# Optimization experiments

Hardware: AMD Instinct MI355X
Metric: run time of the kernel (lower is better)

Reference implementation:

```python
import jax, jax.numpy as jnp
import numpy as np

B, T, D, U = 32, 2048, 512, 512

def setup_inputs() -> dict:
    key = jax.random.key(0)
    ks = jax.random.split(key, 7)
    s = 1.0 / np.sqrt(D)
    return {
        "query": jax.random.normal(ks[0], (B, D), jnp.float32),
        "values": jax.random.normal(ks[1], (B, T, D), jnp.float32),
        "W1": jax.random.normal(ks[2], (D, U), jnp.float32) * s,
        "b1": jnp.zeros((U,), jnp.float32),
        "W2": jax.random.normal(ks[3], (D, U), jnp.float32) * s,
        "b2": jnp.zeros((U,), jnp.float32),
        "V": jax.random.normal(ks[4], (U, 1), jnp.float32) * (1.0 / np.sqrt(U)),
        "bV": jnp.zeros((1,), jnp.float32),
    }

def reference(query, values, W1, b1, W2, b2, V, bV):
    # values: [B,T,D], query: [B,D]
    proj_v = jnp.einsum('btd,du->btu', values, W1) + b1          # [B,T,U]
    proj_q = (query @ W2 + b2)[:, None, :]                        # [B,1,U]
    score = jnp.tanh(proj_v + proj_q) @ V + bV                    # [B,T,1]
    attention_weights = jax.nn.softmax(score, axis=1)             # [B,T,1]
    context_vector = jnp.sum(attention_weights * values, axis=1)  # [B,D]
    return (context_vector, attention_weights)
```

## Files before the change

### kernel.cpp

```cpp
#include <hip/hip_runtime.h>
#include <hip/hip_bf16.h>
#include <math.h>

#define BB 32
#define TT 2048
#define DD 512
#define UU 512

typedef __attribute__((ext_vector_type(8))) short short8v;
typedef __attribute__((ext_vector_type(4))) float floatx4;
typedef __attribute__((ext_vector_type(8))) unsigned short ushort8v;
typedef __attribute__((ext_vector_type(4))) unsigned short ushort4v;

static __device__ inline unsigned short f2bf(float f) {
  __hip_bfloat16 h = __float2bfloat16(f);
  return *reinterpret_cast<unsigned short*>(&h);
}

static __device__ inline float fast_tanh(float x) {
  x = fminf(fmaxf(x, -15.f), 15.f);
  float e2 = __expf(2.f * x);
  return (e2 - 1.f) * __builtin_amdgcn_rcpf(e2 + 1.f);
}

__global__ __launch_bounds__(256) void pack_w1a_kernel(
    const float* __restrict__ W1, unsigned short* __restrict__ w1a) {
  __shared__ float Wf[32][132];
  const int kt = blockIdx.x, uc = blockIdx.y;
  const int tid = threadIdx.x;
  {
    const int k = tid >> 3;
    const int u16 = (tid & 7) * 16;
    const float* src = W1 + (size_t)(kt * 32 + k) * UU + uc * 128 + u16;
    #pragma unroll
    for (int q = 0; q < 4; ++q) {
      const float4 v = *(const float4*)(src + q * 4);
      Wf[k][u16 + q * 4 + 0] = v.x;
      Wf[k][u16 + q * 4 + 1] = v.y;
      Wf[k][u16 + q * 4 + 2] = v.z;
      Wf[k][u16 + q * 4 + 3] = v.w;
    }
  }
  __syncthreads();
  unsigned short* dst = w1a + (size_t)kt * 16384;
  #pragma unroll
  for (int s = 0; s < 2; ++s) {
    const int c = s * 256 + tid;
    const int kg = c >> 7;
    const int u = c & 127;
    ushort8v o;
    #pragma unroll
    for (int e = 0; e < 8; ++e) o[e] = f2bf(Wf[kg * 8 + e][u]);
    *(ushort8v*)(dst + ((size_t)kg * 512 + uc * 128 + u) * 8) = o;
  }
}

__global__ __launch_bounds__(256) void projq_kernel(
    const float* __restrict__ query, const float* __restrict__ W2,
    const float* __restrict__ b2, const float* __restrict__ b1,
    float* __restrict__ qb) {
  int b = blockIdx.x;
  int u = blockIdx.y * 256 + threadIdx.x;
  float acc = b2[u] + b1[u];
  const float* q = query + b * DD;
  #pragma unroll 16
  for (int d = 0; d < DD; ++d) acc += q[d] * W2[(size_t)d * UU + u];
  qb[b * UU + u] = acc;
}

#define SBM 64

__global__ __launch_bounds__(512, 4) void score_fused_kernel(
    const float* __restrict__ values, const unsigned short* __restrict__ w1a,
    const float* __restrict__ qb, const float* __restrict__ V,
    float* __restrict__ score, float* __restrict__ o_part,
    float* __restrict__ l_part) {
  __shared__ __align__(16) unsigned short Bp[2][8][4][SBM][8];
  __shared__ float qv_lds[512];
  __shared__ float vv_lds[512];
  __shared__ float part[8][SBM];
  __shared__ float sw[SBM];
  __shared__ float opart[4][512];

  const int tid = threadIdx.x;
  const int row0 = blockIdx.x * SBM;
  const int b = row0 >> 11;
  const int lane = tid & 63;
  const int wid = tid >> 6;
  const int wu = wid * 64;
  const int fr = lane & 15;
  const int kg = lane >> 4;

  qv_lds[tid] = qb[b * UU + tid];
  vv_lds[tid] = V[tid];

  const int sm = tid >> 3;
  const int sj = tid & 7;
  const float* bsrc = values + (size_t)(row0 + sm) * DD + sj * 4;
  const int bofs = (sj >> 1) * (SBM * 8) + sm * 8 + (sj & 1) * 4;

  {
    float4 r0[8];
    #pragma unroll
    for (int q = 0; q < 8; ++q)
      r0[q] = *(const float4*)(bsrc + (size_t)q * 32);
    #pragma unroll
    for (int q = 0; q < 8; ++q) {
      ushort4v o = {f2bf(r0[q].x), f2bf(r0[q].y), f2bf(r0[q].z), f2bf(r0[q].w)};
      *(ushort4v*)(&Bp[0][q][0][0][0] + bofs) = o;
    }
  }

  const size_t aofs = (size_t)(kg * 512 + wu + fr) * 8;
  short8v af[3][4];
  #pragma unroll
  for (int ju = 0; ju < 4; ++ju) {
    af[0][ju] = *(const short8v*)(w1a + aofs + (size_t)ju * 128);
    af[1][ju] = *(const short8v*)(w1a + 16384 + aofs + (size_t)ju * 128);
  }

  __syncthreads();

  float4 r1[8];
  #pragma unroll
  for (int q = 0; q < 8; ++q)
    r1[q] = *(const float4*)(bsrc + (size_t)(8 + q) * 32);

  floatx4 acc[4][4] = {};

  #pragma unroll
  for (int t = 0; t < 16; ++t) {
    if (t == 8) {
      #pragma unroll
      for (int q = 0; q < 8; ++q) {
        ushort4v o = {f2bf(r1[q].x), f2bf(r1[q].y), f2bf(r1[q].z), f2bf(r1[q].w)};
        *(ushort4v*)(&Bp[1][q][0][0][0] + bofs) = o;
      }
      __syncthreads();
    }

    if (t + 2 < 16) {
      #pragma unroll
      for (int ju = 0; ju < 4; ++ju)
        af[(t + 2) % 3][ju] =
            *(const short8v*)(w1a + (size_t)(t + 2) * 16384 + aofs + (size_t)ju * 128);
    }

    #pragma unroll
    for (int jm = 0; jm < 4; ++jm) {
      const short8v bfv = *(const short8v*)&Bp[t >> 3][t & 7][kg][jm * 16 + fr][0];
      #pragma unroll
      for (int ju = 0; ju < 4; ++ju)
        acc[ju][jm] = __builtin_amdgcn_mfma_f32_16x16x32_bf16(af[t % 3][ju], bfv, acc[ju][jm], 0, 0, 0);
    }
  }

  float pm[4] = {0.f, 0.f, 0.f, 0.f};
  #pragma unroll
  for (int ju = 0; ju < 4; ++ju) {
    const float4 qv = *(const float4*)&qv_lds[wu + ju * 16 + kg * 4];
    const float4 vv = *(const float4*)&vv_lds[wu + ju * 16 + kg * 4];
    const float qa[4] = {qv.x, qv.y, qv.z, qv.w};
    const float va[4] = {vv.x, vv.y, vv.z, vv.w};
    #pragma unroll
    for (int jm = 0; jm < 4; ++jm)
      #pragma unroll
      for (int reg = 0; reg < 4; ++reg)
        pm[jm] += fast_tanh(acc[ju][jm][reg] + qa[reg]) * va[reg];
  }
  #pragma unroll
  for (int jm = 0; jm < 4; ++jm) {
    pm[jm] += __shfl_xor(pm[jm], 16, 64);
    pm[jm] += __shfl_xor(pm[jm], 32, 64);
  }
  if (lane < 16) {
    #pragma unroll
    for (int jm = 0; jm < 4; ++jm) part[wid][jm * 16 + lane] = pm[jm];
  }
  __syncthreads();
  if (tid < SBM) {
    float s = 0.f;
    #pragma unroll
    for (int w = 0; w < 8; ++w) s += part[w][tid];
    score[row0 + tid] = s;
    sw[tid] = __expf(s);
  }
  __syncthreads();

  {
    const int g = tid >> 7;
    const int dq = tid & 127;
    const float* vrow = values + (size_t)(row0 + g * 16) * DD + dq * 4;
    float4 o4 = {0.f, 0.f, 0.f, 0.f};
    #pragma unroll
    for (int r = 0; r < 16; ++r) {
      const float w = sw[g * 16 + r];
      const float4 v = *(const float4*)(vrow + (size_t)r * DD);
      o4.x += w * v.x; o4.y += w * v.y; o4.z += w * v.z; o4.w += w * v.w;
    }
    *(float4*)&opart[g][dq * 4] = o4;
  }
  if (wid == 0) {
    float lv = sw[lane];
    #pragma unroll
    for (int m = 1; m < 64; m <<= 1) lv += __shfl_xor(lv, m, 64);
    if (lane == 0) l_part[blockIdx.x] = lv;
  }
  __syncthreads();
  {
    const int d = tid;
    o_part[(size_t)blockIdx.x * DD + d] =
        opart[0][d] + opart[1][d] + opart[2][d] + opart[3][d];
  }
}

__global__ __launch_bounds__(128) void reduce_kernel(
    const float* __restrict__ o_part, const float* __restrict__ l_part,
    float* __restrict__ ctx, float* __restrict__ Linv) {
  const int b = blockIdx.x;
  const int d0 = threadIdx.x * 4;
  __shared__ float Ls;
  if (threadIdx.x == 0) {
    float s = 0.f;
    #pragma unroll 8
    for (int c = 0; c < 32; ++c) s += l_part[b * 32 + c];
    Ls = 1.f / s;
    Linv[b] = Ls;
  }
  float4 a = {0.f, 0.f, 0.f, 0.f};
  #pragma unroll 8
  for (int c = 0; c < 32; ++c) {
    const float4 p = *(const float4*)(o_part + (size_t)(b * 32 + c) * DD + d0);
    a.x += p.x; a.y += p.y; a.z += p.z; a.w += p.w;
  }
  __syncthreads();
  const float inv = Ls;
  a.x *= inv; a.y *= inv; a.z *= inv; a.w *= inv;
  *(float4*)(ctx + (size_t)b * DD + d0) = a;
}

__global__ __launch_bounds__(1024) void attn_kernel(
    const float* __restrict__ score, const float* __restrict__ Linv,
    float* __restrict__ attn) {
  const int i = blockIdx.x * 1024 + threadIdx.x;
  const int b = i >> 11;
  attn[i] = __expf(score[i]) * Linv[b];
}

extern "C" void kernel_launch(void* const* d_in, const int* in_sizes, int n_in,
                              void* d_out, int out_size, void* d_ws, size_t ws_size,
                              hipStream_t stream) {
  const float* query  = (const float*)d_in[0];
  const float* values = (const float*)d_in[1];
  const float* W1     = (const float*)d_in[2];
  const float* b1     = (const float*)d_in[3];
  const float* W2     = (const float*)d_in[4];
  const float* b2     = (const float*)d_in[5];
  const float* V      = (const float*)d_in[6];

  float* ctx  = (float*)d_out;
  float* attn = (float*)d_out + BB * DD;

  float* qb           = (float*)d_ws;
  float* score        = qb + BB * UU;
  unsigned short* w1a = (unsigned short*)(score + BB * TT);
  float* o_part       = (float*)(w1a + (size_t)UU * DD);
  float* l_part       = o_part + (size_t)1024 * DD;
  float* Linv         = l_part + 1024;

  pack_w1a_kernel<<<dim3(16, 4), 256, 0, stream>>>(W1, w1a);
  projq_kernel<<<dim3(BB, UU / 256), 256, 0, stream>>>(query, W2, b2, b1, qb);

  score_fused_kernel<<<(BB * TT) / SBM, 512, 0, stream>>>(
      values, w1a, qb, V, score, o_part, l_part);

  reduce_kernel<<<BB, 128, 0, stream>>>(o_part, l_part, ctx, Linv);
  attn_kernel<<<(BB * TT) / 1024, 1024, 0, stream>>>(score, Linv, attn);
}
```

Measured before the change: 86.50 us.

## Double score-kernel row tile to 128 and load all values up front

Each block of the fused score kernel now covers 128 rows instead of 64. Every W1 fragment fetched from global memory therefore feeds twice as many MFMAs, which halves W1 traffic per row and halves the number of partial outputs the reduce kernel has to combine. The mid-loop staging of the second half of values is gone: the full K slice is converted to bf16 in LDS before the loop, and the W1 prefetch depth drops from two steps to one. The cost is twice the LDS and accumulator registers per block and occupancy limited to 2 blocks per CU, with no overlap left between the values load and the MFMA work.

```diff
diff --git a/kernel.cpp b/kernel.cpp
--- a/kernel.cpp
+++ b/kernel.cpp
@@ -68,14 +68,14 @@
   qb[b * UU + u] = acc;
 }
 
-#define SBM 64
-
-__global__ __launch_bounds__(512, 4) void score_fused_kernel(
+#define SBM 128
+
+__global__ __launch_bounds__(512, 2) void score_fused_kernel(
     const float* __restrict__ values, const unsigned short* __restrict__ w1a,
     const float* __restrict__ qb, const float* __restrict__ V,
     float* __restrict__ score, float* __restrict__ o_part,
     float* __restrict__ l_part) {
-  __shared__ __align__(16) unsigned short Bp[2][8][4][SBM][8];
+  __shared__ __align__(16) unsigned short Bp[16][4][SBM][8];
   __shared__ float qv_lds[512];
   __shared__ float vv_lds[512];
   __shared__ float part[8][SBM];
@@ -94,68 +94,57 @@
   qv_lds[tid] = qb[b * UU + tid];
   vv_lds[tid] = V[tid];
 
-  const int sm = tid >> 3;
-  const int sj = tid & 7;
-  const float* bsrc = values + (size_t)(row0 + sm) * DD + sj * 4;
-  const int bofs = (sj >> 1) * (SBM * 8) + sm * 8 + (sj & 1) * 4;
-
-  {
-    float4 r0[8];
-    #pragma unroll
-    for (int q = 0; q < 8; ++q)
-      r0[q] = *(const float4*)(bsrc + (size_t)q * 32);
-    #pragma unroll
-    for (int q = 0; q < 8; ++q) {
-      ushort4v o = {f2bf(r0[q].x), f2bf(r0[q].y), f2bf(r0[q].z), f2bf(r0[q].w)};
-      *(ushort4v*)(&Bp[0][q][0][0][0] + bofs) = o;
+  {
+    const int sm = tid >> 2;
+    const int sj = tid & 3;
+    const float* bsrc = values + (size_t)(row0 + sm) * DD + sj * 4;
+    #pragma unroll
+    for (int batch = 0; batch < 4; ++batch) {
+      float4 r[8];
+      #pragma unroll
+      for (int i = 0; i < 8; ++i)
+        r[i] = *(const float4*)(bsrc + (size_t)(batch * 8 + i) * 16);
+      #pragma unroll
+      for (int i = 0; i < 8; ++i) {
+        const int f = sj * 4 + (batch * 8 + i) * 16;
+        const int kt = f >> 5;
+        const int kgw = (f >> 3) & 3;
+        const int e = f & 7;
+        ushort4v o = {f2bf(r[i].x), f2bf(r[i].y), f2bf(r[i].z), f2bf(r[i].w)};
+        *(ushort4v*)&Bp[kt][kgw][sm][e] = o;
+      }
     }
   }
 
   const size_t aofs = (size_t)(kg * 512 + wu + fr) * 8;
-  short8v af[3][4];
-  #pragma unroll
-  for (int ju = 0; ju < 4; ++ju) {
+  short8v af[2][4];
+  #pragma unroll
+  for (int ju = 0; ju < 4; ++ju)
     af[0][ju] = *(const short8v*)(w1a + aofs + (size_t)ju * 128);
-    af[1][ju] = *(const short8v*)(w1a + 16384 + aofs + (size_t)ju * 128);
-  }
-
-  __syncthreads();
-
-  float4 r1[8];
-  #pragma unroll
-  for (int q = 0; q < 8; ++q)
-    r1[q] = *(const float4*)(bsrc + (size_t)(8 + q) * 32);
-
-  floatx4 acc[4][4] = {};
+
+  __syncthreads();
+
+  floatx4 acc[4][8] = {};
 
   #pragma unroll
   for (int t = 0; t < 16; ++t) {
-    if (t == 8) {
-      #pragma unroll
-      for (int q = 0; q < 8; ++q) {
-        ushort4v o = {f2bf(r1[q].x), f2bf(r1[q].y), f2bf(r1[q].z), f2bf(r1[q].w)};
-        *(ushort4v*)(&Bp[1][q][0][0][0] + bofs) = o;
-      }
-      __syncthreads();
-    }
-
-    if (t + 2 < 16) {
+    const int cur = t & 1;
+    if (t + 1 < 16) {
       #pragma unroll
       for (int ju = 0; ju < 4; ++ju)
-        af[(t + 2) % 3][ju] =
-            *(const short8v*)(w1a + (size_t)(t + 2) * 16384 + aofs + (size_t)ju * 128);
-    }
-
-    #pragma unroll
-    for (int jm = 0; jm < 4; ++jm) {
-      const short8v bfv = *(const short8v*)&Bp[t >> 3][t & 7][kg][jm * 16 + fr][0];
+        af[cur ^ 1][ju] =
+            *(const short8v*)(w1a + (size_t)(t + 1) * 16384 + aofs + (size_t)ju * 128);
+    }
+    #pragma unroll
+    for (int jm = 0; jm < 8; ++jm) {
+      const short8v bfv = *(const short8v*)&Bp[t][kg][jm * 16 + fr][0];
       #pragma unroll
       for (int ju = 0; ju < 4; ++ju)
-        acc[ju][jm] = __builtin_amdgcn_mfma_f32_16x16x32_bf16(af[t % 3][ju], bfv, acc[ju][jm], 0, 0, 0);
-    }
-  }
-
-  float pm[4] = {0.f, 0.f, 0.f, 0.f};
+        acc[ju][jm] = __builtin_amdgcn_mfma_f32_16x16x32_bf16(af[cur][ju], bfv, acc[ju][jm], 0, 0, 0);
+    }
+  }
+
+  float pm[8] = {};
   #pragma unroll
   for (int ju = 0; ju < 4; ++ju) {
     const float4 qv = *(const float4*)&qv_lds[wu + ju * 16 + kg * 4];
@@ -163,19 +152,19 @@
     const float qa[4] = {qv.x, qv.y, qv.z, qv.w};
     const float va[4] = {vv.x, vv.y, vv.z, vv.w};
     #pragma unroll
-    for (int jm = 0; jm < 4; ++jm)
+    for (int jm = 0; jm < 8; ++jm)
       #pragma unroll
       for (int reg = 0; reg < 4; ++reg)
         pm[jm] += fast_tanh(acc[ju][jm][reg] + qa[reg]) * va[reg];
   }
   #pragma unroll
-  for (int jm = 0; jm < 4; ++jm) {
+  for (int jm = 0; jm < 8; ++jm) {
     pm[jm] += __shfl_xor(pm[jm], 16, 64);
     pm[jm] += __shfl_xor(pm[jm], 32, 64);
   }
   if (lane < 16) {
     #pragma unroll
-    for (int jm = 0; jm < 4; ++jm) part[wid][jm * 16 + lane] = pm[jm];
+    for (int jm = 0; jm < 8; ++jm) part[wid][jm * 16 + lane] = pm[jm];
   }
   __syncthreads();
   if (tid < SBM) {
@@ -190,18 +179,18 @@
   {
     const int g = tid >> 7;
     const int dq = tid & 127;
-    const float* vrow = values + (size_t)(row0 + g * 16) * DD + dq * 4;
+    const float* vrow = values + (size_t)(row0 + g * 32) * DD + dq * 4;
     float4 o4 = {0.f, 0.f, 0.f, 0.f};
-    #pragma unroll
-    for (int r = 0; r < 16; ++r) {
-      const float w = sw[g * 16 + r];
+    #pragma unroll 8
+    for (int r = 0; r < 32; ++r) {
+      const float w = sw[g * 32 + r];
       const float4 v = *(const float4*)(vrow + (size_t)r * DD);
       o4.x += w * v.x; o4.y += w * v.y; o4.z += w * v.z; o4.w += w * v.w;
     }
     *(float4*)&opart[g][dq * 4] = o4;
   }
   if (wid == 0) {
-    float lv = sw[lane];
+    float lv = sw[lane] + sw[lane + 64];
     #pragma unroll
     for (int m = 1; m < 64; m <<= 1) lv += __shfl_xor(lv, m, 64);
     if (lane == 0) l_part[blockIdx.x] = lv;
@@ -222,15 +211,15 @@
   __shared__ float Ls;
   if (threadIdx.x == 0) {
     float s = 0.f;
-    #pragma unroll 8
-    for (int c = 0; c < 32; ++c) s += l_part[b * 32 + c];
+    #pragma unroll
+    for (int c = 0; c < 16; ++c) s += l_part[b * 16 + c];
     Ls = 1.f / s;
     Linv[b] = Ls;
   }
   float4 a = {0.f, 0.f, 0.f, 0.f};
-  #pragma unroll 8
-  for (int c = 0; c < 32; ++c) {
-    const float4 p = *(const float4*)(o_part + (size_t)(b * 32 + c) * DD + d0);
+  #pragma unroll
+  for (int c = 0; c < 16; ++c) {
+    const float4 p = *(const float4*)(o_part + (size_t)(b * 16 + c) * DD + d0);
     a.x += p.x; a.y += p.y; a.z += p.z; a.w += p.w;
   }
   __syncthreads();
@@ -265,8 +254,8 @@
   float* score        = qb + BB * UU;
   unsigned short* w1a = (unsigned short*)(score + BB * TT);
   float* o_part       = (float*)(w1a + (size_t)UU * DD);
-  float* l_part       = o_part + (size_t)1024 * DD;
-  float* Linv         = l_part + 1024;
+  float* l_part       = o_part + (size_t)512 * DD;
+  float* Linv         = l_part + 512;
 
   pack_w1a_kernel<<<dim3(16, 4), 256, 0, stream>>>(W1, w1a);
   projq_kernel<<<dim3(BB, UU / 256), 256, 0, stream>>>(query, W2, b2, b1, qb);
```

After: 93.86 us. +8.5%, slower.

## Stream values tile per k-step with double-buffered LDS and per-step barriers

Applied to the files above, without the earlier changes.

Replaces the two large half-tile LDS staging phases with a per-k-step double buffer. A 3-deep register ring prefetches the values chunks, and a lightweight sync (lgkmcnt wait plus s_barrier with scheduling fences) runs each step. This cuts LDS footprint from 64KB to 8KB for the B tile, which may raise occupancy, and it spreads global loads across the loop. The cost is 15 workgroup barriers per tile instead of two, and each load has less latency-hiding distance.

```diff
diff --git a/kernel.cpp b/kernel.cpp
--- a/kernel.cpp
+++ b/kernel.cpp
@@ -21,6 +21,14 @@
   x = fminf(fmaxf(x, -15.f), 15.f);
   float e2 = __expf(2.f * x);
   return (e2 - 1.f) * __builtin_amdgcn_rcpf(e2 + 1.f);
+}
+
+static __device__ inline void step_sync() {
+  __builtin_amdgcn_sched_barrier(0);
+  asm volatile("s_waitcnt lgkmcnt(0)" ::: "memory");
+  __builtin_amdgcn_sched_barrier(0);
+  __builtin_amdgcn_s_barrier();
+  __builtin_amdgcn_sched_barrier(0);
 }
 
 __global__ __launch_bounds__(256) void pack_w1a_kernel(
@@ -75,7 +83,7 @@
     const float* __restrict__ qb, const float* __restrict__ V,
     float* __restrict__ score, float* __restrict__ o_part,
     float* __restrict__ l_part) {
-  __shared__ __align__(16) unsigned short Bp[2][8][4][SBM][8];
+  __shared__ __align__(16) unsigned short Bs[2][4][SBM][8];
   __shared__ float qv_lds[512];
   __shared__ float vv_lds[512];
   __shared__ float part[8][SBM];
@@ -99,60 +107,54 @@
   const float* bsrc = values + (size_t)(row0 + sm) * DD + sj * 4;
   const int bofs = (sj >> 1) * (SBM * 8) + sm * 8 + (sj & 1) * 4;
 
-  {
-    float4 r0[8];
-    #pragma unroll
-    for (int q = 0; q < 8; ++q)
-      r0[q] = *(const float4*)(bsrc + (size_t)q * 32);
-    #pragma unroll
-    for (int q = 0; q < 8; ++q) {
-      ushort4v o = {f2bf(r0[q].x), f2bf(r0[q].y), f2bf(r0[q].z), f2bf(r0[q].w)};
-      *(ushort4v*)(&Bp[0][q][0][0][0] + bofs) = o;
-    }
-  }
-
   const size_t aofs = (size_t)(kg * 512 + wu + fr) * 8;
+
+  floatx4 acc[4][4] = {};
   short8v af[3][4];
+  float4 br[3];
+
+  br[0] = *(const float4*)(bsrc);
+  br[1] = *(const float4*)(bsrc + 32);
+  br[2] = *(const float4*)(bsrc + 64);
   #pragma unroll
   for (int ju = 0; ju < 4; ++ju) {
     af[0][ju] = *(const short8v*)(w1a + aofs + (size_t)ju * 128);
     af[1][ju] = *(const short8v*)(w1a + 16384 + aofs + (size_t)ju * 128);
   }
-
-  __syncthreads();
-
-  float4 r1[8];
-  #pragma unroll
-  for (int q = 0; q < 8; ++q)
-    r1[q] = *(const float4*)(bsrc + (size_t)(8 + q) * 32);
-
-  floatx4 acc[4][4] = {};
+  {
+    ushort4v q4 = {f2bf(br[0].x), f2bf(br[0].y), f2bf(br[0].z), f2bf(br[0].w)};
+    *(ushort4v*)((unsigned short*)&Bs[0][0][0][0] + bofs) = q4;
+  }
+  step_sync();
 
   #pragma unroll
   for (int t = 0; t < 16; ++t) {
-    if (t == 8) {
-      #pragma unroll
-      for (int q = 0; q < 8; ++q) {
-        ushort4v o = {f2bf(r1[q].x), f2bf(r1[q].y), f2bf(r1[q].z), f2bf(r1[q].w)};
-        *(ushort4v*)(&Bp[1][q][0][0][0] + bofs) = o;
-      }
-      __syncthreads();
-    }
-
+    const int cur = t & 1;
+    const int nxt = cur ^ 1;
+
+    if (t + 3 < 16)
+      br[t % 3] = *(const float4*)(bsrc + (size_t)(t + 3) * 32);
     if (t + 2 < 16) {
       #pragma unroll
       for (int ju = 0; ju < 4; ++ju)
         af[(t + 2) % 3][ju] =
             *(const short8v*)(w1a + (size_t)(t + 2) * 16384 + aofs + (size_t)ju * 128);
     }
+    if (t + 1 < 16) {
+      const float4 bb = br[(t + 1) % 3];
+      ushort4v q4 = {f2bf(bb.x), f2bf(bb.y), f2bf(bb.z), f2bf(bb.w)};
+      *(ushort4v*)((unsigned short*)&Bs[nxt][0][0][0] + bofs) = q4;
+    }
 
     #pragma unroll
     for (int jm = 0; jm < 4; ++jm) {
-      const short8v bfv = *(const short8v*)&Bp[t >> 3][t & 7][kg][jm * 16 + fr][0];
+      const short8v bfv = *(const short8v*)&Bs[cur][kg][jm * 16 + fr][0];
       #pragma unroll
       for (int ju = 0; ju < 4; ++ju)
         acc[ju][jm] = __builtin_amdgcn_mfma_f32_16x16x32_bf16(af[t % 3][ju], bfv, acc[ju][jm], 0, 0, 0);
     }
+
+    if (t < 15) step_sync();
   }
 
   float pm[4] = {0.f, 0.f, 0.f, 0.f};
```

Measured after the change: 88.78 us. +2.6%, slower.

## Reuse LDS bf16 values for context sum and merge small kernels

Applied to the files above, without the earlier changes.

The context accumulation now reads the bf16 copy of the values tile already staged in shared memory for the MFMA stage, instead of reading the fp32 rows from global memory a second time. This is meant to remove a second pass over the large values tensor. The trade-off is that the context is now computed from bf16-rounded values, which lowers accuracy. Separately, the W1 packing and query-projection kernels are merged into one launch, and the reduce and attention-normalisation kernels are merged into another, which cuts launch count.

```diff
diff --git a/kernel.cpp b/kernel.cpp
--- a/kernel.cpp
+++ b/kernel.cpp
@@ -17,55 +17,62 @@
   return *reinterpret_cast<unsigned short*>(&h);
 }
 
+static __device__ inline float bf2f(unsigned short u) {
+  union { unsigned int i; float f; } x;
+  x.i = ((unsigned int)u) << 16;
+  return x.f;
+}
+
 static __device__ inline float fast_tanh(float x) {
   x = fminf(fmaxf(x, -15.f), 15.f);
   float e2 = __expf(2.f * x);
   return (e2 - 1.f) * __builtin_amdgcn_rcpf(e2 + 1.f);
 }
 
-__global__ __launch_bounds__(256) void pack_w1a_kernel(
-    const float* __restrict__ W1, unsigned short* __restrict__ w1a) {
-  __shared__ float Wf[32][132];
-  const int kt = blockIdx.x, uc = blockIdx.y;
-  const int tid = threadIdx.x;
-  {
-    const int k = tid >> 3;
-    const int u16 = (tid & 7) * 16;
-    const float* src = W1 + (size_t)(kt * 32 + k) * UU + uc * 128 + u16;
-    #pragma unroll
-    for (int q = 0; q < 4; ++q) {
-      const float4 v = *(const float4*)(src + q * 4);
-      Wf[k][u16 + q * 4 + 0] = v.x;
-      Wf[k][u16 + q * 4 + 1] = v.y;
-      Wf[k][u16 + q * 4 + 2] = v.z;
-      Wf[k][u16 + q * 4 + 3] = v.w;
-    }
-  }
-  __syncthreads();
-  unsigned short* dst = w1a + (size_t)kt * 16384;
-  #pragma unroll
-  for (int s = 0; s < 2; ++s) {
-    const int c = s * 256 + tid;
-    const int kg = c >> 7;
-    const int u = c & 127;
-    ushort8v o;
-    #pragma unroll
-    for (int e = 0; e < 8; ++e) o[e] = f2bf(Wf[kg * 8 + e][u]);
-    *(ushort8v*)(dst + ((size_t)kg * 512 + uc * 128 + u) * 8) = o;
-  }
-}
-
-__global__ __launch_bounds__(256) void projq_kernel(
+__global__ __launch_bounds__(256) void prep_kernel(
+    const float* __restrict__ W1, unsigned short* __restrict__ w1a,
     const float* __restrict__ query, const float* __restrict__ W2,
     const float* __restrict__ b2, const float* __restrict__ b1,
     float* __restrict__ qb) {
-  int b = blockIdx.x;
-  int u = blockIdx.y * 256 + threadIdx.x;
-  float acc = b2[u] + b1[u];
-  const float* q = query + b * DD;
-  #pragma unroll 16
-  for (int d = 0; d < DD; ++d) acc += q[d] * W2[(size_t)d * UU + u];
-  qb[b * UU + u] = acc;
+  __shared__ float Wf[32][132];
+  const int tid = threadIdx.x;
+  if (blockIdx.x < 64) {
+    const int kt = blockIdx.x & 15, uc = blockIdx.x >> 4;
+    {
+      const int k = tid >> 3;
+      const int u16 = (tid & 7) * 16;
+      const float* src = W1 + (size_t)(kt * 32 + k) * UU + uc * 128 + u16;
+      #pragma unroll
+      for (int q = 0; q < 4; ++q) {
+        const float4 v = *(const float4*)(src + q * 4);
+        Wf[k][u16 + q * 4 + 0] = v.x;
+        Wf[k][u16 + q * 4 + 1] = v.y;
+        Wf[k][u16 + q * 4 + 2] = v.z;
+        Wf[k][u16 + q * 4 + 3] = v.w;
+      }
+    }
+    __syncthreads();
+    unsigned short* dst = w1a + (size_t)kt * 16384;
+    #pragma unroll
+    for (int s = 0; s < 2; ++s) {
+      const int c = s * 256 + tid;
+      const int kg = c >> 7;
+      const int u = c & 127;
+      ushort8v o;
+      #pragma unroll
+      for (int e = 0; e < 8; ++e) o[e] = f2bf(Wf[kg * 8 + e][u]);
+      *(ushort8v*)(dst + ((size_t)kg * 512 + uc * 128 + u) * 8) = o;
+    }
+  } else {
+    const int bidx = blockIdx.x - 64;
+    const int b = bidx >> 1;
+    const int u = (bidx & 1) * 256 + tid;
+    float acc = b2[u] + b1[u];
+    const float* q = query + b * DD;
+    #pragma unroll 16
+    for (int d = 0; d < DD; ++d) acc += q[d] * W2[(size_t)d * UU + u];
+    qb[b * UU + u] = acc;
+  }
 }
 
 #define SBM 64
@@ -190,13 +197,20 @@
   {
     const int g = tid >> 7;
     const int dq = tid & 127;
-    const float* vrow = values + (size_t)(row0 + g * 16) * DD + dq * 4;
+    const int half = dq >> 6;
+    const int ktl = (dq >> 3) & 7;
+    const int kgl = (dq >> 1) & 3;
+    const int e = (dq & 1) * 4;
     float4 o4 = {0.f, 0.f, 0.f, 0.f};
     #pragma unroll
     for (int r = 0; r < 16; ++r) {
-      const float w = sw[g * 16 + r];
-      const float4 v = *(const float4*)(vrow + (size_t)r * DD);
-      o4.x += w * v.x; o4.y += w * v.y; o4.z += w * v.z; o4.w += w * v.w;
+      const int m = g * 16 + r;
+      const float w = sw[m];
+      const ushort4v v4 = *(const ushort4v*)&Bp[half][ktl][kgl][m][e];
+      o4.x += w * bf2f(v4[0]);
+      o4.y += w * bf2f(v4[1]);
+      o4.z += w * bf2f(v4[2]);
+      o4.w += w * bf2f(v4[3]);
     }
     *(float4*)&opart[g][dq * 4] = o4;
   }
@@ -214,37 +228,39 @@
   }
 }
 
-__global__ __launch_bounds__(128) void reduce_kernel(
+__global__ __launch_bounds__(128) void finish_kernel(
     const float* __restrict__ o_part, const float* __restrict__ l_part,
-    float* __restrict__ ctx, float* __restrict__ Linv) {
-  const int b = blockIdx.x;
-  const int d0 = threadIdx.x * 4;
-  __shared__ float Ls;
-  if (threadIdx.x == 0) {
-    float s = 0.f;
+    const float* __restrict__ score, float* __restrict__ ctx,
+    float* __restrict__ attn) {
+  if (blockIdx.x < 32) {
+    const int b = blockIdx.x;
+    const int d0 = threadIdx.x * 4;
+    float Ls = 0.f;
     #pragma unroll 8
-    for (int c = 0; c < 32; ++c) s += l_part[b * 32 + c];
-    Ls = 1.f / s;
-    Linv[b] = Ls;
-  }
-  float4 a = {0.f, 0.f, 0.f, 0.f};
-  #pragma unroll 8
-  for (int c = 0; c < 32; ++c) {
-    const float4 p = *(const float4*)(o_part + (size_t)(b * 32 + c) * DD + d0);
-    a.x += p.x; a.y += p.y; a.z += p.z; a.w += p.w;
-  }
-  __syncthreads();
-  const float inv = Ls;
-  a.x *= inv; a.y *= inv; a.z *= inv; a.w *= inv;
-  *(float4*)(ctx + (size_t)b * DD + d0) = a;
-}
-
-__global__ __launch_bounds__(1024) void attn_kernel(
-    const float* __restrict__ score, const float* __restrict__ Linv,
-    float* __restrict__ attn) {
-  const int i = blockIdx.x * 1024 + threadIdx.x;
-  const int b = i >> 11;
-  attn[i] = __expf(score[i]) * Linv[b];
+    for (int c = 0; c < 32; ++c) Ls += l_part[b * 32 + c];
+    const float inv = 1.f / Ls;
+    float4 a = {0.f, 0.f, 0.f, 0.f};
+    #pragma unroll 8
+    for (int c = 0; c < 32; ++c) {
+      const float4 p = *(const float4*)(o_part + (size_t)(b * 32 + c) * DD + d0);
+      a.x += p.x; a.y += p.y; a.z += p.z; a.w += p.w;
+    }
+    a.x *= inv; a.y *= inv; a.z *= inv; a.w *= inv;
+    *(float4*)(ctx + (size_t)b * DD + d0) = a;
+  } else {
+    const int c = blockIdx.x - 32;
+    const int b = c >> 1;
+    float Ls = 0.f;
+    #pragma unroll 8
+    for (int q = 0; q < 32; ++q) Ls += l_part[b * 32 + q];
+    const float inv = 1.f / Ls;
+    const int base = c * 1024 + threadIdx.x;
+    #pragma unroll
+    for (int q = 0; q < 8; ++q) {
+      const int i = base + q * 128;
+      attn[i] = __expf(score[i]) * inv;
+    }
+  }
 }
 
 extern "C" void kernel_launch(void* const* d_in, const int* in_sizes, int n_in,
@@ -266,14 +282,11 @@
   unsigned short* w1a = (unsigned short*)(score + BB * TT);
   float* o_part       = (float*)(w1a + (size_t)UU * DD);
   float* l_part       = o_part + (size_t)1024 * DD;
-  float* Linv         = l_part + 1024;
-
-  pack_w1a_kernel<<<dim3(16, 4), 256, 0, stream>>>(W1, w1a);
-  projq_kernel<<<dim3(BB, UU / 256), 256, 0, stream>>>(query, W2, b2, b1, qb);
+
+  prep_kernel<<<128, 256, 0, stream>>>(W1, w1a, query, W2, b2, b1, qb);
 
   score_fused_kernel<<<(BB * TT) / SBM, 512, 0, stream>>>(
       values, w1a, qb, V, score, o_part, l_part);
 
-  reduce_kernel<<<BB, 128, 0, stream>>>(o_part, l_part, ctx, Linv);
-  attn_kernel<<<(BB * TT) / 1024, 1024, 0, stream>>>(score, Linv, attn);
-}
+  finish_kernel<<<96, 128, 0, stream>>>(o_part, l_part, score, ctx, attn);
+}
```

Result: faster. 80.31 us (-7.1%).
